# Performance work log

Hardware: AMD Instinct MI355X
Metric: run time of the kernel (lower is better)

The kernel has to match this reference:

```python
import jax, jax.numpy as jnp
import numpy as np

N_NODES = 100000
N_EDGES = 3200000
IN_F = 500
HID = 64
OUT_F = 64
ALPHA = 0.1
K = 10


def setup_inputs() -> dict:
    key = jax.random.key(0)
    ks = jax.random.split(key, 8)
    x = jax.random.normal(ks[0], (N_NODES, IN_F), dtype=jnp.float32)
    edge_src = jax.random.randint(ks[1], (N_EDGES,), 0, N_NODES, dtype=jnp.int32)
    edge_dst = jax.random.randint(ks[2], (N_EDGES,), 0, N_NODES, dtype=jnp.int32)
    edge_weight = jax.random.uniform(ks[3], (N_EDGES,), dtype=jnp.float32)
    W1 = jax.random.normal(ks[4], (IN_F, HID), dtype=jnp.float32) * (1.0 / np.sqrt(IN_F))
    b1 = jnp.zeros((HID,), dtype=jnp.float32)
    W2 = jax.random.normal(ks[5], (HID, OUT_F), dtype=jnp.float32) * (1.0 / np.sqrt(HID))
    b2 = jnp.zeros((OUT_F,), dtype=jnp.float32)
    return {"x": x, "edge_src": edge_src, "edge_dst": edge_dst,
            "edge_weight": edge_weight, "W1": W1, "b1": b1, "W2": W2, "b2": b2}


def _spmm(edge_src, edge_dst, edge_weight, z):
    # sparse adj @ z : gather rows at src, scale by edge weight, scatter-add at dst
    msg = edge_weight[:, None] * z[edge_src]          # [E, C]
    return jax.ops.segment_sum(msg, edge_dst, num_segments=N_NODES)


def reference(x, edge_src, edge_dst, edge_weight, W1, b1, W2, b2):
    # MLP encoder (dropout is identity at inference)
    h = jax.nn.relu(x @ W1 + b1) @ W2 + b2            # [N, OUT_F]
    # APPNP propagation: z_{k+1} = (1-alpha) * A z_k + alpha * h
    z = h
    for _ in range(K):
        z = (1.0 - ALPHA) * _spmm(edge_src, edge_dst, edge_weight, z) + ALPHA * h
    return z
```

## Files before the change

### kernel.cpp

```cpp
#include <hip/hip_runtime.h>

#define N_NODES 100000
#define N_EDGES 3200000
#define IN_F 500
#define HID 64
#define OUT_F 64
#define ALPHA 0.1f
#define K_ITERS 10
#define SCAN_B ((N_NODES + 255) / 256)

#define NPART 8
#define PART_N (N_NODES / NPART)
#define FILL_GRID 2048

#define KPAD 512

typedef unsigned short ushort_t;
typedef unsigned int uint_t;
typedef int iv4 __attribute__((ext_vector_type(4)));
typedef __attribute__((ext_vector_type(8))) short bf16x8;
typedef __attribute__((ext_vector_type(4))) float f32x4;

__device__ __forceinline__ float bf2f(ushort_t v) {
    union { uint_t u; float f; } c; c.u = ((uint_t)v) << 16; return c.f;
}
__device__ __forceinline__ ushort_t f2b(float f) {
    union { float f; uint_t u; } c; c.f = f;
    uint_t u = c.u + 0x7fffu + ((c.u >> 16) & 1u);
    return (ushort_t)(u >> 16);
}
__device__ __forceinline__ float bflo(uint_t u) {
    union { uint_t u; float f; } c; c.u = u << 16; return c.f;
}
__device__ __forceinline__ float bfhi(uint_t u) {
    union { uint_t u; float f; } c; c.u = u & 0xffff0000u; return c.f;
}
__device__ __forceinline__ uint_t packbf(float a, float b) {
    return (uint_t)f2b(a) | ((uint_t)f2b(b) << 16);
}
__device__ __forceinline__ bf16x8 pack8(float4 a, float4 b) {
    bf16x8 r;
    r[0] = (short)f2b(a.x); r[1] = (short)f2b(a.y);
    r[2] = (short)f2b(a.z); r[3] = (short)f2b(a.w);
    r[4] = (short)f2b(b.x); r[5] = (short)f2b(b.y);
    r[6] = (short)f2b(b.z); r[7] = (short)f2b(b.w);
    return r;
}

__global__ __launch_bounds__(256) void prep_weights(
    const float* __restrict__ W1, const float* __restrict__ W2,
    ushort_t* __restrict__ w1t, ushort_t* __restrict__ w2t)
{
    int i = blockIdx.x * 256 + threadIdx.x;
    if (i < 64 * KPAD) {
        int c = i >> 9, k = i & (KPAD - 1);
        float v = (k < IN_F) ? W1[k * HID + c] : 0.f;
        w1t[c * KPAD + k] = f2b(v);
    } else {
        int j = i - 64 * KPAD;
        if (j < 64 * 64) {
            int c = j >> 6, k = j & 63;
            w2t[c * 64 + k] = f2b(W2[k * OUT_F + c]);
        }
    }
}

__global__ __launch_bounds__(256) void mlp_mfma(
    const float* __restrict__ x, const ushort_t* __restrict__ w1t,
    const float* __restrict__ b1, const ushort_t* __restrict__ w2t,
    const float* __restrict__ b2, ushort_t* __restrict__ hb,
    ushort_t* __restrict__ ahb)
{
    __shared__ ushort_t hs[4][16][64];

    const int lane = threadIdx.x & 63;
    const int wid  = threadIdx.x >> 6;
    const int r16  = lane & 15;
    const int kg   = lane >> 4;
    const int rowbase = blockIdx.x * 64 + wid * 16;

    int arow  = rowbase + r16;
    int lrow  = (arow < N_NODES) ? arow : (N_NODES - 1);
    const float* xr = x + (long)lrow * IN_F;

    f32x4 acc[4];
    #pragma unroll
    for (int t = 0; t < 4; ++t) acc[t] = (f32x4){0.f, 0.f, 0.f, 0.f};

    for (int ks = 0; ks < KPAD / 32; ++ks) {
        const int k0 = ks * 32 + kg * 8;
        bf16x8 af;
        if (k0 + 8 <= IN_F) {
            float4 xa = *(const float4*)(xr + k0);
            float4 xb = *(const float4*)(xr + k0 + 4);
            af = pack8(xa, xb);
        } else {
            #pragma unroll
            for (int i = 0; i < 8; ++i) {
                float v = (k0 + i < IN_F) ? xr[k0 + i] : 0.f;
                af[i] = (short)f2b(v);
            }
        }
        #pragma unroll
        for (int t = 0; t < 4; ++t) {
            bf16x8 bfw = *(const bf16x8*)&w1t[(t * 16 + r16) * KPAD + k0];
            acc[t] = __builtin_amdgcn_mfma_f32_16x16x32_bf16(af, bfw, acc[t], 0, 0, 0);
        }
    }

    #pragma unroll
    for (int t = 0; t < 4; ++t) {
        float bb = b1[t * 16 + r16];
        #pragma unroll
        for (int r = 0; r < 4; ++r) {
            float h = fmaxf(acc[t][r] + bb, 0.f);
            hs[wid][kg * 4 + r][t * 16 + r16] = f2b(h);
        }
    }
    __syncthreads();

    f32x4 acc2[4];
    #pragma unroll
    for (int t = 0; t < 4; ++t) acc2[t] = (f32x4){0.f, 0.f, 0.f, 0.f};

    #pragma unroll
    for (int ks = 0; ks < 2; ++ks) {
        bf16x8 ha = *(const bf16x8*)&hs[wid][r16][ks * 32 + kg * 8];
        #pragma unroll
        for (int t = 0; t < 4; ++t) {
            bf16x8 wb = *(const bf16x8*)&w2t[(t * 16 + r16) * 64 + ks * 32 + kg * 8];
            acc2[t] = __builtin_amdgcn_mfma_f32_16x16x32_bf16(ha, wb, acc2[t], 0, 0, 0);
        }
    }

    #pragma unroll
    for (int t = 0; t < 4; ++t) {
        float bb = b2[t * 16 + r16];
        #pragma unroll
        for (int r = 0; r < 4; ++r) {
            int orow = rowbase + kg * 4 + r;
            if (orow < N_NODES) {
                float v = acc2[t][r] + bb;
                hb[orow * 64 + t * 16 + r16]  = f2b(v);
                ahb[orow * 64 + t * 16 + r16] = f2b(ALPHA * v);
            }
        }
    }
}

__global__ __launch_bounds__(256) void zero_cnt(int* __restrict__ cnt)
{
    int i = blockIdx.x * 256 + threadIdx.x;
    if (i < N_NODES) cnt[i] = 0;
}

__global__ __launch_bounds__(256) void count_keys(
    const int* __restrict__ key, int* __restrict__ cnt)
{
    int i = blockIdx.x * 256 + threadIdx.x;
    if (i < N_EDGES) atomicAdd(&cnt[key[i]], 1);
}

__global__ __launch_bounds__(256) void scan_block_sums(
    const int* __restrict__ cnt, int* __restrict__ bsum)
{
    int i = blockIdx.x * 256 + threadIdx.x;
    int v = (i < N_NODES) ? cnt[i] : 0;
    for (int off = 32; off; off >>= 1) v += __shfl_down(v, off);
    __shared__ int ws_[4];
    if ((threadIdx.x & 63) == 0) ws_[threadIdx.x >> 6] = v;
    __syncthreads();
    if (threadIdx.x == 0) bsum[blockIdx.x] = ws_[0] + ws_[1] + ws_[2] + ws_[3];
}

__global__ __launch_bounds__(512) void scan_partials(
    const int* __restrict__ bsum, int* __restrict__ boff)
{
    int t = threadIdx.x;
    int v = (t < SCAN_B) ? bsum[t] : 0;
    int lane = t & 63, w = t >> 6;
    int x = v;
    for (int off = 1; off < 64; off <<= 1) {
        int y = __shfl_up(x, off);
        if (lane >= off) x += y;
    }
    __shared__ int wsum[8];
    if (lane == 63) wsum[w] = x;
    __syncthreads();
    if (w == 0) {
        int s = (lane < 8) ? wsum[lane] : 0;
        for (int off = 1; off < 8; off <<= 1) {
            int y = __shfl_up(s, off);
            if (lane >= off) s += y;
        }
        if (lane < 8) wsum[lane] = s;
    }
    __syncthreads();
    int wpre = (w == 0) ? 0 : wsum[w - 1];
    if (t < SCAN_B) boff[t] = wpre + x - v;
}

__global__ __launch_bounds__(256) void scan_final(
    const int* __restrict__ cnt, const int* __restrict__ boff,
    int* __restrict__ row_start, int* __restrict__ pos)
{
    int i = blockIdx.x * 256 + threadIdx.x;
    int v = (i < N_NODES) ? cnt[i] : 0;
    int lane = threadIdx.x & 63, w = threadIdx.x >> 6;
    int x = v;
    for (int off = 1; off < 64; off <<= 1) {
        int y = __shfl_up(x, off);
        if (lane >= off) x += y;
    }
    __shared__ int wsum[4];
    if (lane == 63) wsum[w] = x;
    __syncthreads();
    int wpre = 0;
    for (int ww = 0; ww < w; ++ww) wpre += wsum[ww];
    int excl = wpre + x - v;
    int r = boff[blockIdx.x] + excl;
    if (i < N_NODES) { row_start[i] = r; pos[i] = r; }
    if (i == 0) row_start[N_NODES] = N_EDGES;
}

__global__ __launch_bounds__(256) void fill_dst_part(
    const int* __restrict__ esrc, const int* __restrict__ edst,
    const float* __restrict__ ew, int* __restrict__ pos,
    int2* __restrict__ csr)
{
    const int part = blockIdx.x & (NPART - 1);
    const int lo = part * PART_N;
    const int hi = lo + PART_N;
    const int pthreads = (FILL_GRID / NPART) * 256;
    const int NQUAD = N_EDGES / 4;

    for (int qd = (blockIdx.x >> 3) * 256 + threadIdx.x; qd < NQUAD; qd += pthreads) {
        iv4 d4 = __builtin_nontemporal_load((const iv4*)edst + qd);
        const int i0 = qd * 4;
#define DO_EDGE(DV, IDX) do {                                        \
        int d_ = (DV);                                               \
        if (d_ >= lo && d_ < hi) {                                   \
            int   s_ = __builtin_nontemporal_load(&esrc[IDX]);       \
            float w_ = __builtin_nontemporal_load(&ew[IDX]);         \
            int   q_ = atomicAdd(&pos[d_], 1);                       \
            csr[q_] = make_int2(s_, __float_as_int(0.9f * w_));      \
        } } while (0)
        DO_EDGE(d4.x, i0 + 0);
        DO_EDGE(d4.y, i0 + 1);
        DO_EDGE(d4.z, i0 + 2);
        DO_EDGE(d4.w, i0 + 3);
#undef DO_EDGE
    }
}

__global__ __launch_bounds__(256) void sort_rows(
    const int* __restrict__ row_start, int2* __restrict__ csr)
{
    const int node = blockIdx.x * 4 + (threadIdx.x >> 6);
    const int lane = threadIdx.x & 63;
    const int s0 = row_start[node];
    const int s1 = row_start[node + 1];
    int n = s1 - s0; if (n > 64) n = 64;
    int key = 0x7fffffff;
    int val = 0;
    if (lane < n) { int2 e = csr[s0 + lane]; key = e.x; val = e.y; }
    #pragma unroll
    for (int k = 2; k <= 64; k <<= 1) {
        #pragma unroll
        for (int j = k >> 1; j > 0; j >>= 1) {
            int pk = __shfl_xor(key, j, 64);
            int pv = __shfl_xor(val, j, 64);
            bool lower   = (lane & j) == 0;
            bool asc     = (lane & k) == 0;
            bool takeMin = (lower == asc);
            bool pick    = takeMin ? (pk < key) : (pk > key);
            if (pick) { key = pk; val = pv; }
        }
    }
    if (lane < n) csr[s0 + lane] = make_int2(key, val);
}

template <bool FINAL>
__global__ __launch_bounds__(256) void spmm_kernel(
    const int* __restrict__ row_start, const int2* __restrict__ csr,
    const ushort_t* __restrict__ zin, const ushort_t* __restrict__ ahb,
    void* __restrict__ zout)
{
    const int node = blockIdx.x * 4 + (threadIdx.x >> 6);
    const int lane = threadIdx.x & 63;
    const int g = lane >> 3;
    const int q = lane & 7;
    const int s0 = __builtin_amdgcn_readfirstlane(row_start[node]);
    const int s1 = __builtin_amdgcn_readfirstlane(row_start[node + 1]);

    float a0=0.f,a1=0.f,a2=0.f,a3=0.f,a4=0.f,a5=0.f,a6=0.f,a7=0.f;
    if (g == 0) {
        uint4 t = *(const uint4*)&ahb[node * 64 + 8 * q];
        a0 = bflo(t.x); a1 = bfhi(t.x); a2 = bflo(t.y); a3 = bfhi(t.y);
        a4 = bflo(t.z); a5 = bfhi(t.z); a6 = bflo(t.w); a7 = bfhi(t.w);
    }

#define FMA8(WV, ZV) do { \
        a0 = fmaf((WV), bflo((ZV).x), a0); a1 = fmaf((WV), bfhi((ZV).x), a1); \
        a2 = fmaf((WV), bflo((ZV).y), a2); a3 = fmaf((WV), bfhi((ZV).y), a3); \
        a4 = fmaf((WV), bflo((ZV).z), a4); a5 = fmaf((WV), bfhi((ZV).z), a5); \
        a6 = fmaf((WV), bflo((ZV).w), a6); a7 = fmaf((WV), bfhi((ZV).w), a7); \
    } while (0)

    int j = s0;
    for (; j + 32 <= s1; j += 32) {
        int2 e0 = csr[j + g];
        int2 e1 = csr[j + 8 + g];
        int2 e2 = csr[j + 16 + g];
        int2 e3 = csr[j + 24 + g];
        uint4 z0 = *(const uint4*)&zin[e0.x * 64 + 8 * q];
        uint4 z1 = *(const uint4*)&zin[e1.x * 64 + 8 * q];
        uint4 z2 = *(const uint4*)&zin[e2.x * 64 + 8 * q];
        uint4 z3 = *(const uint4*)&zin[e3.x * 64 + 8 * q];
        float w0 = __int_as_float(e0.y);
        float w1 = __int_as_float(e1.y);
        float w2 = __int_as_float(e2.y);
        float w3 = __int_as_float(e3.y);
        FMA8(w0, z0);
        FMA8(w1, z1);
        FMA8(w2, z2);
        FMA8(w3, z3);
    }
    for (; j < s1; j += 8) {
        int2 e = make_int2(0, 0);
        int jj = j + g;
        if (jj < s1) e = csr[jj];
        uint4 zt = *(const uint4*)&zin[e.x * 64 + 8 * q];
        float wt = __int_as_float(e.y);
        FMA8(wt, zt);
    }
#undef FMA8

    #pragma unroll
    for (int m = 8; m <= 32; m <<= 1) {
        a0 += __shfl_xor(a0, m, 64); a1 += __shfl_xor(a1, m, 64);
        a2 += __shfl_xor(a2, m, 64); a3 += __shfl_xor(a3, m, 64);
        a4 += __shfl_xor(a4, m, 64); a5 += __shfl_xor(a5, m, 64);
        a6 += __shfl_xor(a6, m, 64); a7 += __shfl_xor(a7, m, 64);
    }

    if (g == 0) {
        if (FINAL) {
            float* op = (float*)zout + node * 64 + 8 * q;
            *(float4*)op       = make_float4(a0, a1, a2, a3);
            *(float4*)(op + 4) = make_float4(a4, a5, a6, a7);
        } else {
            uint4 pk;
            pk.x = packbf(a0, a1); pk.y = packbf(a2, a3);
            pk.z = packbf(a4, a5); pk.w = packbf(a6, a7);
            *(uint4*)&((ushort_t*)zout)[node * 64 + 8 * q] = pk;
        }
    }
}

extern "C" void kernel_launch(void* const* d_in, const int* in_sizes, int n_in,
                              void* d_out, int out_size, void* d_ws, size_t ws_size,
                              hipStream_t stream)
{
    const float* x    = (const float*)d_in[0];
    const int*   esrc = (const int*)d_in[1];
    const int*   edst = (const int*)d_in[2];
    const float* ew   = (const float*)d_in[3];
    const float* W1   = (const float*)d_in[4];
    const float* b1   = (const float*)d_in[5];
    const float* W2   = (const float*)d_in[6];
    const float* b2   = (const float*)d_in[7];
    float* out = (float*)d_out;

    char* p = (char*)d_ws;
    ushort_t* ahb = (ushort_t*)p;  p += (size_t)N_NODES * 64 * 2;
    ushort_t* hb  = (ushort_t*)p;  p += (size_t)N_NODES * 64 * 2;
    ushort_t* zB  = (ushort_t*)p;  p += (size_t)N_NODES * 64 * 2;
    int2*  csr     = (int2*)p;     p += (size_t)N_EDGES * 8;
    int* cnt       = (int*)p;      p += (size_t)N_NODES * 4;
    int* pos       = (int*)p;      p += (size_t)N_NODES * 4;
    int* row_start = (int*)p;      p += (size_t)(N_NODES + 1) * 4;
    int* bsum      = (int*)p;      p += (size_t)SCAN_B * 4;
    int* boff      = (int*)p;      p += (size_t)SCAN_B * 4;
    ushort_t* w1t  = (ushort_t*)p; p += (size_t)64 * KPAD * 2;
    ushort_t* w2t  = (ushort_t*)p; p += (size_t)64 * 64 * 2;

    const int EB = (N_EDGES + 255) / 256;

    hipLaunchKernelGGL(prep_weights, dim3((64 * KPAD + 64 * 64 + 255) / 256),
                       dim3(256), 0, stream, W1, W2, w1t, w2t);
    hipLaunchKernelGGL(mlp_mfma, dim3((N_NODES + 63) / 64), dim3(256), 0, stream,
                       x, w1t, b1, w2t, b2, hb, ahb);

    hipLaunchKernelGGL(zero_cnt, dim3(SCAN_B), dim3(256), 0, stream, cnt);
    hipLaunchKernelGGL(count_keys, dim3(EB), dim3(256), 0, stream, edst, cnt);
    hipLaunchKernelGGL(scan_block_sums, dim3(SCAN_B), dim3(256), 0, stream, cnt, bsum);
    hipLaunchKernelGGL(scan_partials, dim3(1), dim3(512), 0, stream, bsum, boff);
    hipLaunchKernelGGL(scan_final, dim3(SCAN_B), dim3(256), 0, stream,
                       cnt, boff, row_start, pos);
    hipLaunchKernelGGL(fill_dst_part, dim3(FILL_GRID), dim3(256), 0, stream,
                       esrc, edst, ew, pos, csr);
    hipLaunchKernelGGL(sort_rows, dim3(N_NODES / 4), dim3(256), 0, stream,
                       row_start, csr);

    const ushort_t* zi = hb;
    for (int it = 0; it < K_ITERS - 1; ++it) {
        ushort_t* zo = (it % 2 == 0) ? zB : hb;
        hipLaunchKernelGGL((spmm_kernel<false>), dim3(N_NODES / 4), dim3(256), 0, stream,
                           row_start, csr, zi, ahb, (void*)zo);
        zi = zo;
    }
    hipLaunchKernelGGL((spmm_kernel<true>), dim3(N_NODES / 4), dim3(256), 0, stream,
                       row_start, csr, zi, ahb, (void*)out);
}
```

Baseline: 1.317 ms.

## Replace per-partition edge rescans with a two-pass bucket split and fill

Before, each of the 8 destination partitions rescanned the whole edge list, filtered by destination range, and atomically placed matching edges into the CSR. Now a split_edges kernel reads every edge once and uses wave ballots plus block and global atomics to scatter edges into per-partition buckets, packing the local destination index with the source. A fill_b kernel then reads only its own partition's bucket to build the CSR. The bucket buffer reuses the hidden-feature workspace, so the MLP launch is moved after CSR construction. This adds an extra write and read of the edge stream in exchange for removing the repeated reads of the destination array.

Measured after the change: 1.316 ms. About the same (-0.1%).

```diff
diff --git a/kernel.cpp b/kernel.cpp
--- a/kernel.cpp
+++ b/kernel.cpp
@@ -13,11 +13,14 @@
 #define PART_N (N_NODES / NPART)
 #define FILL_GRID 2048
 
+#define SPLIT_CHUNK 2560
+#define SPLIT_ROUNDS 10
+#define SPLIT_GRID (N_EDGES / SPLIT_CHUNK)
+
 #define KPAD 512
 
 typedef unsigned short ushort_t;
 typedef unsigned int uint_t;
-typedef int iv4 __attribute__((ext_vector_type(4)));
 typedef __attribute__((ext_vector_type(8))) short bf16x8;
 typedef __attribute__((ext_vector_type(4))) float f32x4;
 
@@ -202,7 +205,8 @@
 
 __global__ __launch_bounds__(256) void scan_final(
     const int* __restrict__ cnt, const int* __restrict__ boff,
-    int* __restrict__ row_start, int* __restrict__ pos)
+    int* __restrict__ row_start, int* __restrict__ pos,
+    int* __restrict__ pcur)
 {
     int i = blockIdx.x * 256 + threadIdx.x;
     int v = (i < N_NODES) ? cnt[i] : 0;
@@ -219,37 +223,82 @@
     for (int ww = 0; ww < w; ++ww) wpre += wsum[ww];
     int excl = wpre + x - v;
     int r = boff[blockIdx.x] + excl;
-    if (i < N_NODES) { row_start[i] = r; pos[i] = r; }
+    if (i < N_NODES) {
+        row_start[i] = r; pos[i] = r;
+        if ((i % PART_N) == 0) pcur[i / PART_N] = r;
+    }
     if (i == 0) row_start[N_NODES] = N_EDGES;
 }
 
-__global__ __launch_bounds__(256) void fill_dst_part(
+__global__ __launch_bounds__(256) void split_edges(
     const int* __restrict__ esrc, const int* __restrict__ edst,
-    const float* __restrict__ ew, int* __restrict__ pos,
-    int2* __restrict__ csr)
+    const float* __restrict__ ew, int* __restrict__ pcur,
+    int2* __restrict__ sbuf)
+{
+    __shared__ int lbase[NPART];
+    const int tid  = threadIdx.x;
+    const int lane = tid & 63;
+    const int base = blockIdx.x * SPLIT_CHUNK;
+    const unsigned long long below = (lane == 63) ? ~0ull >> 1
+                                                  : (1ull << lane) - 1ull;
+
+    if (tid < NPART) lbase[tid] = 0;
+    __syncthreads();
+
+    int parts[SPLIT_ROUNDS];
+    int dloc[SPLIT_ROUNDS];
+    int myc = 0;
+    #pragma unroll
+    for (int k = 0; k < SPLIT_ROUNDS; ++k) {
+        int d = edst[base + k * 256 + tid];
+        int p = d / PART_N;
+        parts[k] = p;
+        dloc[k]  = d - p * PART_N;
+        #pragma unroll
+        for (int pp = 0; pp < NPART; ++pp) {
+            unsigned long long m = __ballot(p == pp);
+            if (lane == pp) myc += __popcll(m);
+        }
+    }
+    if (lane < NPART) atomicAdd(&lbase[lane], myc);
+    __syncthreads();
+    if (tid < NPART) lbase[tid] = atomicAdd(&pcur[tid], lbase[tid]);
+    __syncthreads();
+
+    #pragma unroll
+    for (int k = 0; k < SPLIT_ROUNDS; ++k) {
+        const int p = parts[k];
+        int slot = 0;
+        #pragma unroll
+        for (int pp = 0; pp < NPART; ++pp) {
+            unsigned long long m = __ballot(p == pp);
+            int b = 0;
+            if (lane == pp) b = atomicAdd(&lbase[pp], __popcll(m));
+            b = __shfl(b, pp, 64);
+            if (p == pp) slot = b + __popcll(m & below);
+        }
+        int i = base + k * 256 + tid;
+        int s = esrc[i];
+        float w = 0.9f * ew[i];
+        sbuf[slot] = make_int2((dloc[k] << 17) | s, __float_as_int(w));
+    }
+}
+
+__global__ __launch_bounds__(256) void fill_b(
+    const int2* __restrict__ sbuf, const int* __restrict__ row_start,
+    int* __restrict__ pos, int2* __restrict__ csr)
 {
     const int part = blockIdx.x & (NPART - 1);
-    const int lo = part * PART_N;
-    const int hi = lo + PART_N;
-    const int pthreads = (FILL_GRID / NPART) * 256;
-    const int NQUAD = N_EDGES / 4;
-
-    for (int qd = (blockIdx.x >> 3) * 256 + threadIdx.x; qd < NQUAD; qd += pthreads) {
-        iv4 d4 = __builtin_nontemporal_load((const iv4*)edst + qd);
-        const int i0 = qd * 4;
-#define DO_EDGE(DV, IDX) do {                                        \
-        int d_ = (DV);                                               \
-        if (d_ >= lo && d_ < hi) {                                   \
-            int   s_ = __builtin_nontemporal_load(&esrc[IDX]);       \
-            float w_ = __builtin_nontemporal_load(&ew[IDX]);         \
-            int   q_ = atomicAdd(&pos[d_], 1);                       \
-            csr[q_] = make_int2(s_, __float_as_int(0.9f * w_));      \
-        } } while (0)
-        DO_EDGE(d4.x, i0 + 0);
-        DO_EDGE(d4.y, i0 + 1);
-        DO_EDGE(d4.z, i0 + 2);
-        DO_EDGE(d4.w, i0 + 3);
-#undef DO_EDGE
+    const int lo_e = row_start[part * PART_N];
+    const int hi_e = row_start[(part + 1) * PART_N];
+    const int stride = (FILL_GRID / NPART) * 256;
+    for (int i = lo_e + (blockIdx.x >> 3) * 256 + (int)threadIdx.x; i < hi_e;
+         i += stride) {
+        int2 e = sbuf[i];
+        int s = e.x & 0x1ffff;
+        int d = part * PART_N + (((unsigned)e.x) >> 17);
+        int q = atomicAdd(&pos[d], 1);
+        csr[q] = make_int2(s, e.y);
     }
 }
 
@@ -382,26 +431,31 @@
     int* row_start = (int*)p;      p += (size_t)(N_NODES + 1) * 4;
     int* bsum      = (int*)p;      p += (size_t)SCAN_B * 4;
     int* boff      = (int*)p;      p += (size_t)SCAN_B * 4;
+    int* pcur      = (int*)p;      p += (size_t)NPART * 4;
     ushort_t* w1t  = (ushort_t*)p; p += (size_t)64 * KPAD * 2;
     ushort_t* w2t  = (ushort_t*)p; p += (size_t)64 * 64 * 2;
+    int2* sbuf = (int2*)ahb;
 
     const int EB = (N_EDGES + 255) / 256;
 
     hipLaunchKernelGGL(prep_weights, dim3((64 * KPAD + 64 * 64 + 255) / 256),
                        dim3(256), 0, stream, W1, W2, w1t, w2t);
-    hipLaunchKernelGGL(mlp_mfma, dim3((N_NODES + 63) / 64), dim3(256), 0, stream,
-                       x, w1t, b1, w2t, b2, hb, ahb);
 
     hipLaunchKernelGGL(zero_cnt, dim3(SCAN_B), dim3(256), 0, stream, cnt);
     hipLaunchKernelGGL(count_keys, dim3(EB), dim3(256), 0, stream, edst, cnt);
     hipLaunchKernelGGL(scan_block_sums, dim3(SCAN_B), dim3(256), 0, stream, cnt, bsum);
     hipLaunchKernelGGL(scan_partials, dim3(1), dim3(512), 0, stream, bsum, boff);
     hipLaunchKernelGGL(scan_final, dim3(SCAN_B), dim3(256), 0, stream,
-                       cnt, boff, row_start, pos);
-    hipLaunchKernelGGL(fill_dst_part, dim3(FILL_GRID), dim3(256), 0, stream,
-                       esrc, edst, ew, pos, csr);
+                       cnt, boff, row_start, pos, pcur);
+    hipLaunchKernelGGL(split_edges, dim3(SPLIT_GRID), dim3(256), 0, stream,
+                       esrc, edst, ew, pcur, sbuf);
+    hipLaunchKernelGGL(fill_b, dim3(FILL_GRID), dim3(256), 0, stream,
+                       sbuf, row_start, pos, csr);
     hipLaunchKernelGGL(sort_rows, dim3(N_NODES / 4), dim3(256), 0, stream,
                        row_start, csr);
+
+    hipLaunchKernelGGL(mlp_mfma, dim3((N_NODES + 63) / 64), dim3(256), 0, stream,
+                       x, w1t, b1, w2t, b2, hb, ahb);
 
     const ushort_t* zi = hb;
     for (int it = 0; it < K_ITERS - 1; ++it) {
```
